# Kernel tuning notes

Hardware: AMD Instinct MI355X
Metric: run time of the kernel (lower is better)

## Reference

```python
import math
import jax, jax.numpy as jnp
import numpy as np

E = 1024
H = 16
DH = E // H
R = 8
ALPHA = 16
LORA_S = ALPHA / R

def build_slopes(h):
    start = 2 ** (-2 ** (-(math.log2(h) - 3)))
    return jnp.asarray([start * start ** i for i in range(h)], dtype=jnp.float32)

def setup_inputs() -> dict:
    key = jax.random.key(0)
    ks = jax.random.split(key, 12)
    B, T = 2, 2048
    x = jax.random.normal(ks[0], (B, T, E), dtype=jnp.float32)
    # nn.Linear weights: [out_f, in_f]; LoRA A: [out_f, r], B: [r, in_f]
    def lin(k):
        return jax.random.normal(k, (E, E), dtype=jnp.float32) / math.sqrt(E)
    inp = {
        "x": x,
        "Wq": lin(ks[1]), "Aq": jax.random.normal(ks[2], (E, R)) * 0.01, "Bq": jax.random.normal(ks[3], (R, E)) * 0.01,
        "Wk": lin(ks[4]), "Ak": jax.random.normal(ks[5], (E, R)) * 0.01, "Bk": jax.random.normal(ks[6], (R, E)) * 0.01,
        "Wv": lin(ks[7]), "Av": jax.random.normal(ks[8], (E, R)) * 0.01, "Bv": jax.random.normal(ks[9], (R, E)) * 0.01,
        "Wp": lin(ks[10]),
    }
    return inp

def _lora(x, W, A, Bm):
    # x @ W.T + (x @ B.T) @ A.T * s
    return x @ W.T + ((x @ Bm.T) @ A.T) * LORA_S

def reference(x, Wq, Aq, Bq, Wk, Ak, Bk, Wv, Av, Bv, Wp):
    B, T, _ = x.shape
    slopes = build_slopes(H)  # [H]
    q = _lora(x, Wq, Aq, Bq).reshape(B, T, H, DH).transpose(0, 2, 1, 3)  # [B,H,T,dh]
    k = _lora(x, Wk, Ak, Bk).reshape(B, T, H, DH).transpose(0, 2, 1, 3)
    v = _lora(x, Wv, Av, Bv).reshape(B, T, H, DH).transpose(0, 2, 1, 3)
    s = jnp.einsum("bhqd,bhkd->bhqk", q, k) / math.sqrt(DH)
    i = jnp.arange(T, dtype=jnp.float32)[:, None]
    j = jnp.arange(T, dtype=jnp.float32)[None, :]
    alibi = slopes[:, None, None] * (i - j)  # [H,T,T]
    mask = jnp.triu(jnp.full((T, T), -jnp.inf, dtype=jnp.float32), 1)
    s = s + alibi[None] + mask
    p = jax.nn.softmax(s, axis=-1)
    o = jnp.einsum("bhqk,bhkd->bhqd", p, v).transpose(0, 2, 1, 3).reshape(B, T, E)
    return o @ Wp.T
```

## Files before the change

### kernel.cpp

```cpp
#include <hip/hip_runtime.h>

typedef unsigned short u16;
typedef unsigned int   u32;
typedef __bf16 bf16_t;
typedef bf16_t bf16x8 __attribute__((ext_vector_type(8)));
typedef bf16_t bf16x2v __attribute__((ext_vector_type(2)));
typedef float  f32x4  __attribute__((ext_vector_type(4)));

#define E_DIM 1024
#define T_DIM 2048
#define H_NUM 16
#define DH 64
#define BT 4096
#define Y_LD 2048

__device__ __forceinline__ u16 f2bf(float f) {
  u32 u = __builtin_bit_cast(u32, f);
  u32 r = (u + 0x7fffu + ((u >> 16) & 1u)) >> 16;
  return (u16)r;
}
__device__ __forceinline__ float bf2f(u16 v) {
  u32 u = ((u32)v) << 16;
  return __builtin_bit_cast(float, u);
}

__device__ __forceinline__ float fexp2(float x) {
#if __has_builtin(__builtin_amdgcn_exp2f)
  return __builtin_amdgcn_exp2f(x);
#else
  return exp2f(x);
#endif
}

__device__ __forceinline__ int swz(int r, int c) {
  return r * 64 + (c ^ ((r & 7) << 3));
}

__device__ __forceinline__ void store_val(float* p, float v) { *p = v; }
__device__ __forceinline__ void store_val(u16* p, float v)   { *p = f2bf(v); }

typedef __attribute__((address_space(3))) unsigned int as3_u32;
typedef const __attribute__((address_space(1))) unsigned int as1_u32;

__device__ __forceinline__ void async16(const u16* g, u16* l) {
  __builtin_amdgcn_global_load_lds((as1_u32*)g, (as3_u32*)l, 16, 0, 0);
}

__device__ __forceinline__ void waitvm0_barrier() {
  asm volatile("s_waitcnt vmcnt(0)" ::: "memory");
  __builtin_amdgcn_s_barrier();
  __builtin_amdgcn_sched_barrier(0);
}

__device__ __forceinline__ u32 pack2(float a, float b) {
  bf16x2v v;
  v[0] = (bf16_t)a;
  v[1] = (bf16_t)b;
  return __builtin_bit_cast(u32, v);
}

__device__ __forceinline__ void plswap(u32& a, u32& b) {
#if __has_builtin(__builtin_amdgcn_permlane32_swap)
  typedef u32 u32x2 __attribute__((ext_vector_type(2)));
  u32x2 r = __builtin_amdgcn_permlane32_swap(a, b, false, false);
  a = r[0];
  b = r[1];
#else
  asm volatile("v_permlane32_swap_b32 %0, %1" : "+v"(a), "+v"(b));
#endif
}

__device__ __forceinline__ void redist_pair(u32 A, u32 B, bool odd, u32& wj, u32& wj2) {
  plswap(A, B);
  u32 sA = __builtin_amdgcn_ds_swizzle(A, 0x401F);
  u32 sB = __builtin_amdgcn_ds_swizzle(B, 0x401F);
  wj  = odd ? sB : A;
  wj2 = odd ? B : sA;
}

__global__ __launch_bounds__(256) void k_prep(
    const float* __restrict__ x,
    const float* __restrict__ W0, const float* __restrict__ A0, const float* __restrict__ B0,
    const float* __restrict__ W1, const float* __restrict__ A1, const float* __restrict__ B1,
    const float* __restrict__ W2, const float* __restrict__ A2, const float* __restrict__ B2,
    const float* __restrict__ Wp,
    u16* __restrict__ xb, u16* __restrict__ Weff, u16* __restrict__ Wpb, float s0) {
  const int blk = blockIdx.x;
  const int tid = threadIdx.x;
  if (blk < 4096) {
    int i = (blk * 256 + tid) * 4;
    float4 v = *reinterpret_cast<const float4*>(x + i);
    u32 lo = (u32)f2bf(v.x) | ((u32)f2bf(v.y) << 16);
    u32 hi = (u32)f2bf(v.z) | ((u32)f2bf(v.w) << 16);
    *reinterpret_cast<uint2*>(xb + i) = make_uint2(lo, hi);
  } else if (blk < 7168) {
    int e4 = (blk - 4096) * 256 + tid;
    int m = e4 >> 18;
    int e = (e4 & 262143) * 4;
    const float* W  = (m == 0) ? W0 : (m == 1) ? W1 : W2;
    const float* A  = (m == 0) ? A0 : (m == 1) ? A1 : A2;
    const float* Bm = (m == 0) ? B0 : (m == 1) ? B1 : B2;
    const float sc  = (m == 0) ? s0 : 1.0f;
    int o = e >> 10, i = e & 1023;
    float4 wv = *reinterpret_cast<const float4*>(W + e);
    float acc[4] = {wv.x, wv.y, wv.z, wv.w};
#pragma unroll
    for (int r = 0; r < 8; ++r) {
      float a2 = 2.0f * A[o * 8 + r];
      float4 bv = *reinterpret_cast<const float4*>(Bm + r * 1024 + i);
      acc[0] += a2 * bv.x; acc[1] += a2 * bv.y; acc[2] += a2 * bv.z; acc[3] += a2 * bv.w;
    }
    u32 lo = (u32)f2bf(acc[0] * sc) | ((u32)f2bf(acc[1] * sc) << 16);
    u32 hi = (u32)f2bf(acc[2] * sc) | ((u32)f2bf(acc[3] * sc) << 16);
    *reinterpret_cast<uint2*>(Weff + (size_t)m * 1048576 + e) = make_uint2(lo, hi);
  } else {
    int i = ((blk - 7168) * 256 + tid) * 4;
    float4 v = *reinterpret_cast<const float4*>(Wp + i);
    u32 lo = (u32)f2bf(v.x) | ((u32)f2bf(v.y) << 16);
    u32 hi = (u32)f2bf(v.z) | ((u32)f2bf(v.w) << 16);
    *reinterpret_cast<uint2*>(Wpb + i) = make_uint2(lo, hi);
  }
}

template <typename OUT_T, bool QKV>
__global__ __launch_bounds__(256) void k_gemm_bt(
    const u16* __restrict__ A, const u16* __restrict__ B,
    OUT_T* __restrict__ C, u16* __restrict__ Vt, int K, int ldc) {
  __shared__ __align__(16) u16 As[128 * 64];
  __shared__ __align__(16) u16 Bs[128 * 64];
  const int tid  = threadIdx.x;
  const int lane = tid & 63;
  const int wave = tid >> 6;
  const int wr = wave >> 1, wc = wave & 1;
  const int m0 = blockIdx.y * 128;
  const int n0 = blockIdx.x * 128;
  const int lr = lane & 15;
  const int lk = (lane >> 4) * 8;
  const bool vmode = QKV && (n0 >= 2048);

  f32x4 acc[4][4] = {};

  for (int k0 = 0; k0 < K; k0 += 64) {
    __syncthreads();
#pragma unroll
    for (int p = 0; p < 4; ++p) {
      const int off = (p * 4 + wave) * 512;
      const int e = off + lane * 8;
      const int r = e >> 6, c = e & 63;
      const int cs = c ^ ((r & 7) << 3);
      async16(&A[(size_t)(m0 + r) * K + k0 + cs], As + off);
      async16(&B[(size_t)(n0 + r) * K + k0 + cs], Bs + off);
    }
    __syncthreads();
#pragma unroll
    for (int kk = 0; kk < 2; ++kk) {
      bf16x8 af[4], bfr[4];
#pragma unroll
      for (int mi = 0; mi < 4; ++mi)
        af[mi] = *reinterpret_cast<const bf16x8*>(&As[swz(wr * 64 + mi * 16 + lr, kk * 32 + lk)]);
#pragma unroll
      for (int ni = 0; ni < 4; ++ni)
        bfr[ni] = *reinterpret_cast<const bf16x8*>(&Bs[swz(wc * 64 + ni * 16 + lr, kk * 32 + lk)]);
      if (vmode) {
#pragma unroll
        for (int mi = 0; mi < 4; ++mi)
#pragma unroll
          for (int ni = 0; ni < 4; ++ni)
            acc[mi][ni] = __builtin_amdgcn_mfma_f32_16x16x32_bf16(bfr[ni], af[mi], acc[mi][ni], 0, 0, 0);
      } else {
#pragma unroll
        for (int mi = 0; mi < 4; ++mi)
#pragma unroll
          for (int ni = 0; ni < 4; ++ni)
            acc[mi][ni] = __builtin_amdgcn_mfma_f32_16x16x32_bf16(af[mi], bfr[ni], acc[mi][ni], 0, 0, 0);
      }
    }
  }
  const int rg = (lane >> 4) * 4;
  if (vmode) {
#pragma unroll
    for (int mi = 0; mi < 4; ++mi)
#pragma unroll
      for (int ni = 0; ni < 4; ++ni)
#pragma unroll
        for (int q = 0; q < 4; ++q) {
          int o = n0 - 2048 + wc * 64 + ni * 16 + rg + q;
          int h = o >> 6, d = o & 63;
          int rowm = m0 + wr * 64 + mi * 16 + lr;
          int b = rowm >> 11, t = rowm & 2047;
          Vt[(size_t)(((b << 4) + h) * 64 + d) * 2048 + t] = f2bf(acc[mi][ni][q]);
        }
  } else {
#pragma unroll
    for (int mi = 0; mi < 4; ++mi)
#pragma unroll
      for (int ni = 0; ni < 4; ++ni)
#pragma unroll
        for (int q = 0; q < 4; ++q) {
          int row = m0 + wr * 64 + mi * 16 + rg + q;
          int col = n0 + wc * 64 + ni * 16 + lr;
          store_val(&C[(size_t)row * ldc + col], acc[mi][ni][q]);
        }
  }
}

__global__ __launch_bounds__(256) void k_attn8(
    const u16* __restrict__ Y, const u16* __restrict__ Vt, u16* __restrict__ Og,
    u16* __restrict__ Oa, u16* __restrict__ Ob,
    float* __restrict__ la, float* __restrict__ lb) {
  __shared__ __align__(16) u16 Ks[2][4096];
  __shared__ __align__(16) u16 Vs[2][4096];

  const int tid = threadIdx.x;
  const int lane = tid & 63;
  const int wave = tid >> 6;
  const int lr = lane & 15;
  const int lg = lane >> 4;
  const int lk = lg * 8;
  const bool odd = (lane & 16) != 0;

  const int orig = blockIdx.x;
  const int bh = orig & 31;
  const int c  = orig >> 5;
  const int qt = (c < 16) ? (16 + c) : (47 - c);
  const int ks = (c >= 16 && c < 32) ? 16 : 0;
  const int ke = (c < 16) ? 15 : qt;
  const int b = bh >> 4, h = bh & 15;

  const float LOG2E = 1.4426950408889634f;
  const float slope2 = exp2f(-0.5f * (float)(h + 1)) * LOG2E;

  const u16* Kb = Y + (size_t)b * T_DIM * Y_LD + 1024 + h * DH;
  const u16* Vb = Vt + (size_t)bh * DH * T_DIM;

  bf16x8 qf[2];
  {
    const int qrow = qt * 64 + wave * 16 + lr;
#pragma unroll
    for (int kk = 0; kk < 2; ++kk)
      qf[kk] = *reinterpret_cast<const bf16x8*>(
          &Y[(size_t)(b * T_DIM + qrow) * Y_LD + h * DH + kk * 32 + lk]);
  }

  float nkb[16];
#pragma unroll
  for (int ni = 0; ni < 4; ++ni)
#pragma unroll
    for (int r = 0; r < 4; ++r)
      nkb[ni * 4 + r] = -slope2 * (float)(ni * 16 + lg * 4 + r) - 12.0f;

  bf16x8 ones;
#pragma unroll
  for (int jj = 0; jj < 8; ++jj) ones[jj] = (bf16_t)1.0f;

  f32x4 oacc[4] = {};
  f32x4 lacc = {};

  auto stage = [&](int bufi, int kt) {
    const int kv0 = kt * 64;
#pragma unroll
    for (int q = 0; q < 2; ++q) {
      const int off = (q * 4 + wave) * 512;
      const int e = off + lane * 8;
      const int r = e >> 6, cc = e & 63;
      const int cs = cc ^ ((r & 7) << 3);
      async16(Kb + (size_t)(kv0 + r) * Y_LD + cs, &Ks[bufi][off]);
      async16(Vb + (size_t)r * T_DIM + kv0 + cs, &Vs[bufi][off]);
    }
  };

  auto step = [&](int kt, int buf, bool DIAG) {
    f32x4 s[4] = {};
    __builtin_amdgcn_s_setprio(1);
#pragma unroll
    for (int kk = 0; kk < 2; ++kk)
#pragma unroll
      for (int ni = 0; ni < 4; ++ni) {
        bf16x8 kf = *reinterpret_cast<const bf16x8*>(&Ks[buf][swz(ni * 16 + lr, kk * 32 + lk)]);
        s[ni] = __builtin_amdgcn_mfma_f32_16x16x32_bf16(kf, qf[kk], s[ni], 0, 0, 0);
      }
    __builtin_amdgcn_s_setprio(0);
    const float ck = -slope2 * (float)(kt * 64);
    u32 pk[4][2];
#pragma unroll
    for (int ni = 0; ni < 4; ++ni) {
      float p[4];
#pragma unroll
      for (int r = 0; r < 4; ++r) {
        float sc = s[ni][r] + nkb[ni * 4 + r] + ck;
        if (DIAG && (ni * 16 + lg * 4 + r) > (wave * 16 + lr)) sc = -INFINITY;
        p[r] = fexp2(sc);
      }
      pk[ni][0] = pack2(p[0], p[1]);
      pk[ni][1] = pack2(p[2], p[3]);
    }
    uint4 PW[2];
#pragma unroll
    for (int kk = 0; kk < 2; ++kk) {
      redist_pair(pk[2 * kk][0], pk[2 * kk + 1][0], odd, PW[kk].x, PW[kk].z);
      redist_pair(pk[2 * kk][1], pk[2 * kk + 1][1], odd, PW[kk].y, PW[kk].w);
    }
    __builtin_amdgcn_s_setprio(1);
#pragma unroll
    for (int kk = 0; kk < 2; ++kk) {
      bf16x8 ph = __builtin_bit_cast(bf16x8, PW[kk]);
      lacc = __builtin_amdgcn_mfma_f32_16x16x32_bf16(ph, ones, lacc, 0, 0, 0);
#pragma unroll
      for (int f = 0; f < 4; ++f) {
        bf16x8 vf = *reinterpret_cast<const bf16x8*>(&Vs[buf][swz(f * 16 + lr, kk * 32 + lk)]);
        oacc[f] = __builtin_amdgcn_mfma_f32_16x16x32_bf16(ph, vf, oacc[f], 0, 0, 0);
      }
    }
    __builtin_amdgcn_s_setprio(0);
  };

  stage(0, ks);
  waitvm0_barrier();
  int buf = 0;
  for (int kt = ks; kt <= ke; ++kt) {
    if (kt < ke) stage(buf ^ 1, kt + 1);
    step(kt, buf, kt == qt);
    waitvm0_barrier();
    buf ^= 1;
  }

  if (c >= 32) {
    float linv[4];
#pragma unroll
    for (int r = 0; r < 4; ++r) linv[r] = 1.0f / lacc[r];
#pragma unroll
    for (int f = 0; f < 4; ++f)
#pragma unroll
      for (int r = 0; r < 4; ++r) {
        int q = qt * 64 + wave * 16 + lg * 4 + r;
        Og[(size_t)(b * T_DIM + q) * E_DIM + h * DH + f * 16 + lr] =
            f2bf(oacc[f][r] * linv[r]);
      }
  } else {
    u16* Op   = (c < 16) ? Oa : Ob;
    float* lp = (c < 16) ? la : lb;
#pragma unroll
    for (int f = 0; f < 4; ++f)
#pragma unroll
      for (int r = 0; r < 4; ++r) {
        int q = qt * 64 + wave * 16 + lg * 4 + r;
        Op[(size_t)(b * 1024 + (q - 1024)) * E_DIM + h * DH + f * 16 + lr] =
            f2bf(oacc[f][r]);
      }
    if (lr == 0) {
#pragma unroll
      for (int r = 0; r < 4; ++r) {
        int q = qt * 64 + wave * 16 + lg * 4 + r;
        lp[bh * 1024 + (q - 1024)] = lacc[r];
      }
    }
  }
}

__global__ __launch_bounds__(256) void k_merge(
    const u16* __restrict__ Oa, const u16* __restrict__ Ob,
    const float* __restrict__ la, const float* __restrict__ lb,
    u16* __restrict__ Og) {
  int idx = blockIdx.x * 256 + threadIdx.x;
  int row = idx >> 8;
  int cg  = (idx & 255) * 4;
  int b = row >> 10, tl = row & 1023;
  int h = cg >> 6;
  size_t po = (size_t)row * E_DIM + cg;
  uint2 ua = *reinterpret_cast<const uint2*>(Oa + po);
  uint2 ub = *reinterpret_cast<const uint2*>(Ob + po);
  float l = la[((b << 4) + h) * 1024 + tl] + lb[((b << 4) + h) * 1024 + tl];
  float inv = 1.0f / l;
  const u16* pa = reinterpret_cast<const u16*>(&ua);
  const u16* pb = reinterpret_cast<const u16*>(&ub);
  u16 o[4];
#pragma unroll
  for (int j = 0; j < 4; ++j)
    o[j] = f2bf((bf2f(pa[j]) + bf2f(pb[j])) * inv);
  *reinterpret_cast<uint2*>(Og + (size_t)(b * T_DIM + 1024 + tl) * E_DIM + cg) =
      *reinterpret_cast<const uint2*>(o);
}

extern "C" void kernel_launch(void* const* d_in, const int* in_sizes, int n_in,
                              void* d_out, int out_size, void* d_ws, size_t ws_size,
                              hipStream_t stream) {
  const float* x  = (const float*)d_in[0];
  const float* Wq = (const float*)d_in[1];
  const float* Aq = (const float*)d_in[2];
  const float* Bq = (const float*)d_in[3];
  const float* Wk = (const float*)d_in[4];
  const float* Ak = (const float*)d_in[5];
  const float* Bk = (const float*)d_in[6];
  const float* Wv = (const float*)d_in[7];
  const float* Av = (const float*)d_in[8];
  const float* Bv = (const float*)d_in[9];
  const float* Wp = (const float*)d_in[10];
  float* out = (float*)d_out;

  char* ws = (char*)d_ws;
  const size_t MB = 1048576;
  u16* xb   = (u16*)(ws);
  u16* Oa   = (u16*)(ws);
  u16* Ob   = (u16*)(ws + 4 * MB);
  u16* Weff = (u16*)(ws + 8 * MB);
  float* la = (float*)(ws + 8 * MB);
  float* lb = (float*)(ws + 8 * MB + 131072);
  u16* Yq   = (u16*)(ws + 14 * MB);
  u16* VtB  = (u16*)(ws + 30 * MB);
  u16* Wpb  = (u16*)(ws + 38 * MB);
  u16* Og   = (u16*)(ws + 40 * MB);

  const float ISQ2 = 0.125f * 1.4426950408889634f;

  k_prep<<<8192, 256, 0, stream>>>(x, Wq, Aq, Bq, Wk, Ak, Bk, Wv, Av, Bv, Wp,
                                   xb, Weff, Wpb, ISQ2);
  {
    dim3 grid(24, 32);
    k_gemm_bt<u16, true><<<grid, 256, 0, stream>>>(xb, Weff, Yq, VtB, E_DIM, Y_LD);
  }
  k_attn8<<<1536, 256, 0, stream>>>(Yq, VtB, Og, Oa, Ob, la, lb);
  k_merge<<<2048, 256, 0, stream>>>(Oa, Ob, la, lb, Og);
  {
    dim3 grid(8, 32);
    k_gemm_bt<float, false><<<grid, 256, 0, stream>>>(Og, Wpb, out, nullptr, E_DIM, E_DIM);
  }
}
```

Measured before the change: 112.7 us.

## Double-buffer GEMM LDS tiles and use 8 waves per block

The projection GEMM now uses two LDS buffers so the next K-tile's async loads are issued while MFMAs run on the current tile, replacing the load-then-barrier-then-compute sequence. The block grows to 512 threads (8 waves in a 2x4 grid), each wave owning a 64x32 sub-tile, to give more latency hiding. MFMA sections get raised wave priority. LDS use doubles to 64KB per block, which may limit residency, and each wave gets less register reuse per fragment load.

```diff
diff --git a/kernel.cpp b/kernel.cpp
--- a/kernel.cpp
+++ b/kernel.cpp
@@ -123,68 +123,83 @@
 }
 
 template <typename OUT_T, bool QKV>
-__global__ __launch_bounds__(256) void k_gemm_bt(
+__global__ __launch_bounds__(512) void k_gemm2(
     const u16* __restrict__ A, const u16* __restrict__ B,
     OUT_T* __restrict__ C, u16* __restrict__ Vt, int K, int ldc) {
-  __shared__ __align__(16) u16 As[128 * 64];
-  __shared__ __align__(16) u16 Bs[128 * 64];
+  __shared__ __align__(16) u16 As[2][8192];
+  __shared__ __align__(16) u16 Bs[2][8192];
   const int tid  = threadIdx.x;
   const int lane = tid & 63;
   const int wave = tid >> 6;
-  const int wr = wave >> 1, wc = wave & 1;
+  const int wr = wave >> 2;
+  const int wc = wave & 3;
   const int m0 = blockIdx.y * 128;
   const int n0 = blockIdx.x * 128;
   const int lr = lane & 15;
   const int lk = (lane >> 4) * 8;
   const bool vmode = QKV && (n0 >= 2048);
 
-  f32x4 acc[4][4] = {};
-
-  for (int k0 = 0; k0 < K; k0 += 64) {
-    __syncthreads();
-#pragma unroll
-    for (int p = 0; p < 4; ++p) {
-      const int off = (p * 4 + wave) * 512;
+  f32x4 acc[4][2] = {};
+
+  auto stageg = [&](int bufi, int t) {
+    const int k0 = t * 64;
+#pragma unroll
+    for (int p = 0; p < 2; ++p) {
+      const int off = (p * 8 + wave) * 512;
       const int e = off + lane * 8;
       const int r = e >> 6, c = e & 63;
       const int cs = c ^ ((r & 7) << 3);
-      async16(&A[(size_t)(m0 + r) * K + k0 + cs], As + off);
-      async16(&B[(size_t)(n0 + r) * K + k0 + cs], Bs + off);
-    }
-    __syncthreads();
+      async16(&A[(size_t)(m0 + r) * K + t * 64 + cs], &As[bufi][off]);
+      async16(&B[(size_t)(n0 + r) * K + t * 64 + cs], &Bs[bufi][off]);
+    }
+    (void)k0;
+  };
+
+  const int nt = K >> 6;
+  stageg(0, 0);
+  waitvm0_barrier();
+  int buf = 0;
+
+  for (int t = 0; t < nt; ++t) {
+    if (t + 1 < nt) stageg(buf ^ 1, t + 1);
+    __builtin_amdgcn_s_setprio(1);
 #pragma unroll
     for (int kk = 0; kk < 2; ++kk) {
-      bf16x8 af[4], bfr[4];
+      bf16x8 af[4], bfr[2];
 #pragma unroll
       for (int mi = 0; mi < 4; ++mi)
-        af[mi] = *reinterpret_cast<const bf16x8*>(&As[swz(wr * 64 + mi * 16 + lr, kk * 32 + lk)]);
-#pragma unroll
-      for (int ni = 0; ni < 4; ++ni)
-        bfr[ni] = *reinterpret_cast<const bf16x8*>(&Bs[swz(wc * 64 + ni * 16 + lr, kk * 32 + lk)]);
+        af[mi] = *reinterpret_cast<const bf16x8*>(&As[buf][swz(wr * 64 + mi * 16 + lr, kk * 32 + lk)]);
+#pragma unroll
+      for (int ni = 0; ni < 2; ++ni)
+        bfr[ni] = *reinterpret_cast<const bf16x8*>(&Bs[buf][swz(wc * 32 + ni * 16 + lr, kk * 32 + lk)]);
       if (vmode) {
 #pragma unroll
         for (int mi = 0; mi < 4; ++mi)
 #pragma unroll
-          for (int ni = 0; ni < 4; ++ni)
+          for (int ni = 0; ni < 2; ++ni)
             acc[mi][ni] = __builtin_amdgcn_mfma_f32_16x16x32_bf16(bfr[ni], af[mi], acc[mi][ni], 0, 0, 0);
       } else {
 #pragma unroll
         for (int mi = 0; mi < 4; ++mi)
 #pragma unroll
-          for (int ni = 0; ni < 4; ++ni)
+          for (int ni = 0; ni < 2; ++ni)
             acc[mi][ni] = __builtin_amdgcn_mfma_f32_16x16x32_bf16(af[mi], bfr[ni], acc[mi][ni], 0, 0, 0);
       }
     }
-  }
+    __builtin_amdgcn_s_setprio(0);
+    waitvm0_barrier();
+    buf ^= 1;
+  }
+
   const int rg = (lane >> 4) * 4;
   if (vmode) {
 #pragma unroll
     for (int mi = 0; mi < 4; ++mi)
 #pragma unroll
-      for (int ni = 0; ni < 4; ++ni)
+      for (int ni = 0; ni < 2; ++ni)
 #pragma unroll
         for (int q = 0; q < 4; ++q) {
-          int o = n0 - 2048 + wc * 64 + ni * 16 + rg + q;
+          int o = n0 - 2048 + wc * 32 + ni * 16 + rg + q;
           int h = o >> 6, d = o & 63;
           int rowm = m0 + wr * 64 + mi * 16 + lr;
           int b = rowm >> 11, t = rowm & 2047;
@@ -194,11 +209,11 @@
 #pragma unroll
     for (int mi = 0; mi < 4; ++mi)
 #pragma unroll
-      for (int ni = 0; ni < 4; ++ni)
+      for (int ni = 0; ni < 2; ++ni)
 #pragma unroll
         for (int q = 0; q < 4; ++q) {
           int row = m0 + wr * 64 + mi * 16 + rg + q;
-          int col = n0 + wc * 64 + ni * 16 + lr;
+          int col = n0 + wc * 32 + ni * 16 + lr;
           store_val(&C[(size_t)row * ldc + col], acc[mi][ni][q]);
         }
   }
@@ -416,12 +431,12 @@
                                    xb, Weff, Wpb, ISQ2);
   {
     dim3 grid(24, 32);
-    k_gemm_bt<u16, true><<<grid, 256, 0, stream>>>(xb, Weff, Yq, VtB, E_DIM, Y_LD);
+    k_gemm2<u16, true><<<grid, 512, 0, stream>>>(xb, Weff, Yq, VtB, E_DIM, Y_LD);
   }
   k_attn8<<<1536, 256, 0, stream>>>(Yq, VtB, Og, Oa, Ob, la, lb);
   k_merge<<<2048, 256, 0, stream>>>(Oa, Ob, la, lb, Og);
   {
     dim3 grid(8, 32);
-    k_gemm_bt<float, false><<<grid, 256, 0, stream>>>(Og, Wpb, out, nullptr, E_DIM, E_DIM);
-  }
-}
+    k_gemm2<float, false><<<grid, 512, 0, stream>>>(Og, Wpb, out, nullptr, E_DIM, E_DIM);
+  }
+}
```

Result: faster. 108.7 us (-3.6%).
